# Performance work log

Hardware: AMD Instinct MI355X
Metric: run time of the kernel (lower is better)

Reference implementation:

```python
import jax, jax.numpy as jnp
import numpy as np

N_NODES = 50000
N_EDGES = 600000
D = 128
HIDDEN = 128
N_GRAPHS = 128
N_CLASSES = 10
N_STACKED = 3  # num_layers - 1


def setup_inputs() -> dict:
    key = jax.random.key(0)
    ks = jax.random.split(key, 12)
    s = 1.0 / np.sqrt(HIDDEN)
    inp = {
        "x": jax.random.normal(ks[0], (N_NODES, D), dtype=jnp.float32),
        "edge_index": jax.random.randint(ks[1], (2, N_EDGES), 0, N_NODES, dtype=jnp.int64),
        "batch": jnp.sort(jax.random.randint(ks[2], (N_NODES,), 0, N_GRAPHS, dtype=jnp.int64)),
        "W1": jax.random.normal(ks[3], (D, HIDDEN), dtype=jnp.float32) * s,
        "R1": jax.random.normal(ks[4], (D, HIDDEN), dtype=jnp.float32) * s,
        "b1": jnp.zeros((HIDDEN,), dtype=jnp.float32),
        "Wc": jax.random.normal(ks[5], (N_STACKED, HIDDEN, HIDDEN), dtype=jnp.float32) * s,
        "Rc": jax.random.normal(ks[6], (N_STACKED, HIDDEN, HIDDEN), dtype=jnp.float32) * s,
        "bc": jnp.zeros((N_STACKED, HIDDEN), dtype=jnp.float32),
        "lin1_w": jax.random.normal(ks[7], (HIDDEN, HIDDEN), dtype=jnp.float32) * s,
        "lin1_b": jnp.zeros((HIDDEN,), dtype=jnp.float32),
        "lin2_w": jax.random.normal(ks[8], (HIDDEN, N_CLASSES), dtype=jnp.float32) * s,
        "lin2_b": jnp.zeros((N_CLASSES,), dtype=jnp.float32),
    }
    return inp


def _gcn_norm(edge_index, n_nodes):
    # symmetric GCN normalization coeffs per edge (edge_weight=None -> ones)
    src, dst = edge_index[0], edge_index[1]
    ones = jnp.ones((edge_index.shape[1],), dtype=jnp.float32)
    deg = jax.ops.segment_sum(ones, dst, num_segments=n_nodes)
    dinv = jnp.where(deg > 0, jax.lax.rsqrt(jnp.maximum(deg, 1.0)), 0.0)
    return dinv[src] * dinv[dst]


def _gcs(x, src, dst, norm, W, R, b):
    # GCN aggregation on transformed features + linear skip (root) connection
    h = x @ W                                   # [N, H]
    msg = h[src] * norm[:, None]                # gather + scale, [E, H]
    agg = jax.ops.segment_sum(msg, dst, num_segments=x.shape[0])
    return agg + x @ R + b


def reference(x, edge_index, batch, W1, R1, b1, Wc, Rc, bc,
              lin1_w, lin1_b, lin2_w, lin2_b):
    src, dst = edge_index[0], edge_index[1]
    norm = _gcn_norm(edge_index, x.shape[0])

    h = jax.nn.relu(_gcs(x, src, dst, norm, W1, R1, b1))
    for i in range(N_STACKED):
        h = jax.nn.relu(_gcs(h, src, dst, norm, Wc[i], Rc[i], bc[i]))
    last = h

    # global mean pool over graphs
    sums = jax.ops.segment_sum(h, batch, num_segments=N_GRAPHS)
    cnts = jax.ops.segment_sum(jnp.ones((h.shape[0],), h.dtype), batch,
                               num_segments=N_GRAPHS)
    pooled = sums / jnp.maximum(cnts, 1.0)[:, None]

    g = jax.nn.relu(pooled @ lin1_w + lin1_b)   # dropout is identity in eval mode
    logits = g @ lin2_w + lin2_b
    return jax.nn.log_softmax(logits, axis=-1), last
```

## Files before the change

kernel.cpp:

```cpp
#include <hip/hip_runtime.h>

#define N_NODES  50000
#define N_EDGES  600000
#define DIM      128
#define N_GRAPHS 128
#define N_CLASSES 10
#define NB_SCAN  196


typedef __bf16 bf16x8 __attribute__((ext_vector_type(8)));
typedef float  f32x4  __attribute__((ext_vector_type(4)));

__device__ inline unsigned short f2bf(float f) {
  union { float f; unsigned int i; } u; u.f = f;
  unsigned int r = u.i + 0x7fff + ((u.i >> 16) & 1);
  return (unsigned short)(r >> 16);
}
__device__ inline float bf2f(unsigned short s) {
  union { unsigned int i; float f; } u; u.i = ((unsigned int)s) << 16;
  return u.f;
}
__device__ inline bf16x8 zero8() {
  union { bf16x8 v; unsigned long long q[2]; } u;
  u.q[0] = 0ull; u.q[1] = 0ull;
  return u.v;
}
__device__ inline bf16x8 pack8(float4 lo, float4 hi) {
  union { bf16x8 v; unsigned short s[8]; } u;
  u.s[0] = f2bf(lo.x); u.s[1] = f2bf(lo.y); u.s[2] = f2bf(lo.z); u.s[3] = f2bf(lo.w);
  u.s[4] = f2bf(hi.x); u.s[5] = f2bf(hi.y); u.s[6] = f2bf(hi.z); u.s[7] = f2bf(hi.w);
  return u.v;
}


__global__ __launch_bounds__(256) void k_zero(float* __restrict__ p, int n) {
  int i = blockIdx.x * 256 + threadIdx.x;
  if (i < n) p[i] = 0.f;
}


__global__ __launch_bounds__(256) void k_pack(const float* __restrict__ W1,
                                              const float* __restrict__ R1,
                                              const float* __restrict__ Wc,
                                              const float* __restrict__ Rc,
                                              unsigned short* __restrict__ pk) {
  int mm = blockIdx.y;
  const float* src = (mm == 0) ? W1
                   : (mm < 4)  ? Wc + (size_t)(mm - 1) * DIM * DIM
                   : (mm == 4) ? R1
                               : Rc + (size_t)(mm - 5) * DIM * DIM;
  int idx = blockIdx.x * 256 + threadIdx.x;
  int lane = idx & 63;
  int kc   = (idx >> 6) & 3;
  int nt   = idx >> 8;
  int col  = nt * 16 + (lane & 15);
  int k0   = kc * 32 + (lane >> 4) * 8;
  unsigned short* dst = pk + (size_t)mm * 16384 + (size_t)idx * 8;
  ushort4 u;
  u.x = f2bf(src[(k0 + 0) * DIM + col]);
  u.y = f2bf(src[(k0 + 1) * DIM + col]);
  u.z = f2bf(src[(k0 + 2) * DIM + col]);
  u.w = f2bf(src[(k0 + 3) * DIM + col]);
  *(ushort4*)&dst[0] = u;
  u.x = f2bf(src[(k0 + 4) * DIM + col]);
  u.y = f2bf(src[(k0 + 5) * DIM + col]);
  u.z = f2bf(src[(k0 + 6) * DIM + col]);
  u.w = f2bf(src[(k0 + 7) * DIM + col]);
  *(ushort4*)&dst[4] = u;
}


__global__ __launch_bounds__(256) void k_deg(const int* __restrict__ ei,
                                             int* __restrict__ deg) {
  int e = blockIdx.x * 256 + threadIdx.x;
  if (e < N_EDGES) atomicAdd(&deg[ei[N_EDGES + e]], 1);
}

__global__ __launch_bounds__(256) void k_dinv(const int* __restrict__ deg,
                                              float* __restrict__ dinv) {
  int n = blockIdx.x * 256 + threadIdx.x;
  if (n < N_NODES) {
    int d = deg[n];
    dinv[n] = (d > 0) ? rsqrtf((float)d) : 0.f;
  }
}

__global__ __launch_bounds__(256) void k_bsum(const int* __restrict__ deg,
                                              int* __restrict__ bsum) {
  int i = blockIdx.x * 256 + threadIdx.x;
  int v = (i < N_NODES) ? deg[i] : 0;
  __shared__ int tmp[256];
  int t = threadIdx.x;
  tmp[t] = v;
  __syncthreads();
  for (int off = 128; off > 0; off >>= 1) {
    if (t < off) tmp[t] += tmp[t + off];
    __syncthreads();
  }
  if (t == 0) bsum[blockIdx.x] = tmp[0];
}

__global__ __launch_bounds__(256) void k_bscan(const int* __restrict__ bsum,
                                               int* __restrict__ boff,
                                               int* __restrict__ rowp) {
  int t = threadIdx.x;
  int v = (t < NB_SCAN) ? bsum[t] : 0;
  __shared__ int tmp[256];
  tmp[t] = v;
  __syncthreads();
  for (int off = 1; off < 256; off <<= 1) {
    int add = (t >= off) ? tmp[t - off] : 0;
    __syncthreads();
    tmp[t] += add;
    __syncthreads();
  }
  boff[t] = tmp[t] - v;
  if (t == 0) rowp[N_NODES] = N_EDGES;
}

__global__ __launch_bounds__(256) void k_rowp(const int* __restrict__ deg,
                                              const int* __restrict__ boff,
                                              int* __restrict__ rowp) {
  int i = blockIdx.x * 256 + threadIdx.x;
  int t = threadIdx.x;
  int v = (i < N_NODES) ? deg[i] : 0;
  __shared__ int tmp[256];
  tmp[t] = v;
  __syncthreads();
  for (int off = 1; off < 256; off <<= 1) {
    int add = (t >= off) ? tmp[t - off] : 0;
    __syncthreads();
    tmp[t] += add;
    __syncthreads();
  }
  if (i < N_NODES) rowp[i] = boff[blockIdx.x] + tmp[t] - v;
}

__global__ __launch_bounds__(256) void k_fill(const int* __restrict__ ei,
                                              const int* __restrict__ rowp,
                                              int* __restrict__ cnt,
                                              const float* __restrict__ dinv,
                                              int* __restrict__ csrc,
                                              float* __restrict__ enorm) {
  int e = blockIdx.x * 256 + threadIdx.x;
  if (e < N_EDGES) {
    int s = ei[e];
    int d = ei[N_EDGES + e];
    int p = rowp[d] + atomicAdd(&cnt[d], 1);
    csrc[p] = s;
    enorm[p] = dinv[s] * dinv[d];
  }
}


template<bool AF32, bool LAST>
__global__ __launch_bounds__(256) void k_gemm(const void* __restrict__ act,
                                              const unsigned short* __restrict__ pkW,
                                              const unsigned short* __restrict__ pkR,
                                              const float* __restrict__ bv,
                                              unsigned short* __restrict__ hwb,
                                              unsigned short* __restrict__ skipb,
                                              float* __restrict__ skipf) {
  const int tid  = threadIdx.x;
  const int wave = tid >> 6, lane = tid & 63;
  const int m = lane & 15, q = lane >> 4;
  const int rbase = blockIdx.x * 64 + wave * 16;
  const int arow  = rbase + m;
  const bool aok  = arow < N_NODES;

  bf16x8 a[4];
  if (AF32) {
    const float* xf = (const float*)act;
#pragma unroll
    for (int kc = 0; kc < 4; ++kc) {
      float4 lo = make_float4(0.f, 0.f, 0.f, 0.f);
      float4 hi = make_float4(0.f, 0.f, 0.f, 0.f);
      if (aok) {
        lo = *(const float4*)&xf[arow * DIM + kc * 32 + q * 8];
        hi = *(const float4*)&xf[arow * DIM + kc * 32 + q * 8 + 4];
      }
      a[kc] = pack8(lo, hi);
    }
  } else {
    const unsigned short* xb = (const unsigned short*)act;
#pragma unroll
    for (int kc = 0; kc < 4; ++kc) {
      bf16x8 v = zero8();
      if (aok) v = *(const bf16x8*)&xb[arow * DIM + kc * 32 + q * 8];
      a[kc] = v;
    }
  }

  f32x4 acc[16];
#pragma unroll
  for (int t = 0; t < 16; ++t) acc[t] = (f32x4){0.f, 0.f, 0.f, 0.f};

#pragma unroll
  for (int nt = 0; nt < 8; ++nt) {
    const unsigned short* pw = pkW + ((size_t)(nt * 4) * 64 + lane) * 8;
    const unsigned short* pr = pkR + ((size_t)(nt * 4) * 64 + lane) * 8;
#pragma unroll
    for (int kc = 0; kc < 4; ++kc) {
      bf16x8 bW = *(const bf16x8*)(pw + (size_t)kc * 64 * 8);
      acc[nt] = __builtin_amdgcn_mfma_f32_16x16x32_bf16(a[kc], bW, acc[nt], 0, 0, 0);
    }
#pragma unroll
    for (int kc = 0; kc < 4; ++kc) {
      bf16x8 bR = *(const bf16x8*)(pr + (size_t)kc * 64 * 8);
      acc[8 + nt] = __builtin_amdgcn_mfma_f32_16x16x32_bf16(a[kc], bR, acc[8 + nt], 0, 0, 0);
    }
  }

#pragma unroll
  for (int nt = 0; nt < 8; ++nt) {
    int col = nt * 16 + m;
#pragma unroll
    for (int rg = 0; rg < 4; ++rg) {
      int row = rbase + q * 4 + rg;
      if (row < N_NODES) hwb[row * DIM + col] = f2bf(acc[nt][rg]);
    }
  }
#pragma unroll
  for (int nt = 0; nt < 8; ++nt) {
    int col = nt * 16 + m;
    float bias = bv[col];
#pragma unroll
    for (int rg = 0; rg < 4; ++rg) {
      int row = rbase + q * 4 + rg;
      if (row < N_NODES) {
        float v = acc[8 + nt][rg] + bias;
        if (LAST) skipf[row * DIM + col] = v;
        else      skipb[row * DIM + col] = f2bf(v);
      }
    }
  }
}


template<bool LAST>
__global__ __launch_bounds__(256) void k_agg(const unsigned short* __restrict__ hwb,
                                             const int* __restrict__ rowp,
                                             const int* __restrict__ csrc,
                                             const float* __restrict__ enorm,
                                             unsigned short* __restrict__ actb,
                                             float* __restrict__ actf) {
  int n = blockIdx.x * 8 + (threadIdx.x >> 5);
  if (n >= N_NODES) return;
  int l4 = (threadIdx.x & 31) * 4;
  float4 acc;
  if (LAST) {
    acc = *(const float4*)&actf[n * DIM + l4];
  } else {
    ushort4 s = *(const ushort4*)&actb[n * DIM + l4];
    acc = make_float4(bf2f(s.x), bf2f(s.y), bf2f(s.z), bf2f(s.w));
  }
  int e = rowp[n], e1 = rowp[n + 1];
  for (; e + 4 <= e1; e += 4) {
    int s0 = csrc[e],     s1 = csrc[e + 1], s2 = csrc[e + 2], s3 = csrc[e + 3];
    float w0 = enorm[e],  w1 = enorm[e + 1], w2 = enorm[e + 2], w3 = enorm[e + 3];
    ushort4 u0 = *(const ushort4*)&hwb[s0 * DIM + l4];
    ushort4 u1 = *(const ushort4*)&hwb[s1 * DIM + l4];
    ushort4 u2 = *(const ushort4*)&hwb[s2 * DIM + l4];
    ushort4 u3 = *(const ushort4*)&hwb[s3 * DIM + l4];
    acc.x = fmaf(w0, bf2f(u0.x), fmaf(w1, bf2f(u1.x), fmaf(w2, bf2f(u2.x), fmaf(w3, bf2f(u3.x), acc.x))));
    acc.y = fmaf(w0, bf2f(u0.y), fmaf(w1, bf2f(u1.y), fmaf(w2, bf2f(u2.y), fmaf(w3, bf2f(u3.y), acc.y))));
    acc.z = fmaf(w0, bf2f(u0.z), fmaf(w1, bf2f(u1.z), fmaf(w2, bf2f(u2.z), fmaf(w3, bf2f(u3.z), acc.z))));
    acc.w = fmaf(w0, bf2f(u0.w), fmaf(w1, bf2f(u1.w), fmaf(w2, bf2f(u2.w), fmaf(w3, bf2f(u3.w), acc.w))));
  }
  for (; e < e1; ++e) {
    int s0 = csrc[e];
    float w0 = enorm[e];
    ushort4 u0 = *(const ushort4*)&hwb[s0 * DIM + l4];
    acc.x = fmaf(w0, bf2f(u0.x), acc.x);
    acc.y = fmaf(w0, bf2f(u0.y), acc.y);
    acc.z = fmaf(w0, bf2f(u0.z), acc.z);
    acc.w = fmaf(w0, bf2f(u0.w), acc.w);
  }
  acc.x = fmaxf(acc.x, 0.f);
  acc.y = fmaxf(acc.y, 0.f);
  acc.z = fmaxf(acc.z, 0.f);
  acc.w = fmaxf(acc.w, 0.f);
  if (LAST) {
    *(float4*)&actf[n * DIM + l4] = acc;
  } else {
    ushort4 o;
    o.x = f2bf(acc.x); o.y = f2bf(acc.y); o.z = f2bf(acc.z); o.w = f2bf(acc.w);
    *(ushort4*)&actb[n * DIM + l4] = o;
  }
}


__global__ __launch_bounds__(1024) void k_pool2(const float* __restrict__ h,
                                                const int* __restrict__ batch,
                                                float* __restrict__ pooled) {
  int g = blockIdx.x;
  int t = threadIdx.x;
  __shared__ int sb[2];
  if (t < 2) {
    int target = g + t;
    int lo = 0, hi = N_NODES;
    while (lo < hi) {
      int mid = (lo + hi) >> 1;
      if (batch[mid] < target) lo = mid + 1; else hi = mid;
    }
    sb[t] = lo;
  }
  __syncthreads();
  int start = sb[0], end = sb[1];
  int c = t & 127, rg = t >> 7;
  float acc = 0.f;
  for (int r = start + rg; r < end; r += 8) acc += h[r * DIM + c];
  __shared__ float sp[8][DIM];
  sp[rg][c] = acc;
  __syncthreads();
  if (rg == 0) {
    float tot = acc;
#pragma unroll
    for (int i = 1; i < 8; ++i) tot += sp[i][c];
    float cnt = fmaxf((float)(end - start), 1.f);
    pooled[g * DIM + c] = tot / cnt;
  }
}


__global__ __launch_bounds__(128) void k_mlp1(const float* __restrict__ pooled,
                                              const float* __restrict__ w,
                                              const float* __restrict__ bias,
                                              float* __restrict__ g1) {
  int g = blockIdx.x, t = threadIdx.x;
  __shared__ float sp[DIM];
  sp[t] = pooled[g * DIM + t];
  __syncthreads();
  float acc = bias[t];
#pragma unroll 4
  for (int k = 0; k < DIM; ++k) acc = fmaf(sp[k], w[k * DIM + t], acc);
  g1[g * DIM + t] = fmaxf(acc, 0.f);
}

__global__ __launch_bounds__(128) void k_mlp2(const float* __restrict__ g1,
                                              const float* __restrict__ w,
                                              const float* __restrict__ bias,
                                              float* __restrict__ out) {
  int g = threadIdx.x;
  float l[N_CLASSES];
#pragma unroll
  for (int c = 0; c < N_CLASSES; ++c) l[c] = bias[c];
  for (int k = 0; k < DIM; ++k) {
    float gv = g1[g * DIM + k];
#pragma unroll
    for (int c = 0; c < N_CLASSES; ++c) l[c] = fmaf(gv, w[k * N_CLASSES + c], l[c]);
  }
  float m = l[0];
#pragma unroll
  for (int c = 1; c < N_CLASSES; ++c) m = fmaxf(m, l[c]);
  float s = 0.f;
#pragma unroll
  for (int c = 0; c < N_CLASSES; ++c) s += expf(l[c] - m);
  float lse = logf(s) + m;
#pragma unroll
  for (int c = 0; c < N_CLASSES; ++c) out[g * N_CLASSES + c] = l[c] - lse;
}


extern "C" void kernel_launch(void* const* d_in, const int* in_sizes, int n_in,
                              void* d_out, int out_size, void* d_ws, size_t ws_size,
                              hipStream_t stream) {
  const float* x     = (const float*)d_in[0];
  const int* ei      = (const int*)d_in[1];
  const int* batch   = (const int*)d_in[2];
  const float* W1  = (const float*)d_in[3];
  const float* R1  = (const float*)d_in[4];
  const float* b1  = (const float*)d_in[5];
  const float* Wc  = (const float*)d_in[6];
  const float* Rc  = (const float*)d_in[7];
  const float* bc  = (const float*)d_in[8];
  const float* l1w = (const float*)d_in[9];
  const float* l1b = (const float*)d_in[10];
  const float* l2w = (const float*)d_in[11];
  const float* l2b = (const float*)d_in[12];

  float* out   = (float*)d_out;
  float* dlast = out + N_GRAPHS * N_CLASSES;

  float* ws    = (float*)d_ws;
  unsigned short* hwb  = (unsigned short*)ws;
  unsigned short* actb = (unsigned short*)(ws + 3200000);
  int*   deg   = (int*)(ws + 6400000);
  int*   cnt   = (int*)(ws + 6450000);
  float* pooled= ws + 6500000;
  float* dinv  = ws + 6516384;
  int*   rowp  = (int*)(ws + 6566384);
  int*   csrc  = (int*)(ws + 6616400);
  float* enorm = ws + 7216400;
  float* g1    = ws + 7816400;
  unsigned short* pk = (unsigned short*)(ws + 7832784);
  int*   bsum  = (int*)(ws + 7898320);
  int*   boff  = (int*)(ws + 7898576);

  k_zero<<<(100000 + 255) / 256, 256, 0, stream>>>(ws + 6400000, 100000);

  k_pack<<<dim3(8, 8), 256, 0, stream>>>(W1, R1, Wc, Rc, pk);
  k_deg <<<(N_EDGES + 255) / 256, 256, 0, stream>>>(ei, deg);
  k_dinv<<<(N_NODES + 255) / 256, 256, 0, stream>>>(deg, dinv);
  k_bsum<<<NB_SCAN, 256, 0, stream>>>(deg, bsum);
  k_bscan<<<1, 256, 0, stream>>>(bsum, boff, rowp);
  k_rowp<<<NB_SCAN, 256, 0, stream>>>(deg, boff, rowp);
  k_fill<<<(N_EDGES + 255) / 256, 256, 0, stream>>>(ei, rowp, cnt, dinv, csrc, enorm);

  const int NGB = (N_NODES + 63) / 64;
  const int NAB = (N_NODES + 7) / 8;

  k_gemm<true, false><<<NGB, 256, 0, stream>>>(
      x, pk + 0 * 16384, pk + 4 * 16384, b1, hwb, actb, nullptr);
  k_agg<false><<<NAB, 256, 0, stream>>>(hwb, rowp, csrc, enorm, actb, nullptr);

  for (int l = 1; l <= 2; ++l) {
    k_gemm<false, false><<<NGB, 256, 0, stream>>>(
        actb, pk + (size_t)l * 16384, pk + (size_t)(4 + l) * 16384,
        bc + (size_t)(l - 1) * DIM, hwb, actb, nullptr);
    k_agg<false><<<NAB, 256, 0, stream>>>(hwb, rowp, csrc, enorm, actb, nullptr);
  }

  k_gemm<false, true><<<NGB, 256, 0, stream>>>(
      actb, pk + 3 * 16384, pk + 7 * 16384, bc + 2 * DIM, hwb, nullptr, dlast);
  k_agg<true><<<NAB, 256, 0, stream>>>(hwb, rowp, csrc, enorm, nullptr, dlast);

  k_pool2<<<N_GRAPHS, 1024, 0, stream>>>(dlast, batch, pooled);
  k_mlp1<<<N_GRAPHS, 128, 0, stream>>>(pooled, l1w, l1b, g1);
  k_mlp2<<<1, N_GRAPHS, 0, stream>>>(g1, l2w, l2b, out);
}
```

Measured before the change: 402.8 us.

## Fuse aggregation into next layer's GEMM and pad CSR rows to four edges

Each layer's neighbor aggregation (plus skip, bias, ReLU) is now done inside the following GEMM kernel, with the result staged in LDS. This removes the round trip of the activation tensor through global memory and cuts the number of launches, using ping-pong h buffers and a separate skip buffer. CSR rows are padded to multiples of four with zero-filled csrc/enorm entries so the edge loop can use int4/float4 loads with no scalar tail. Zeroing, weight packing and the dinv/bsum kernels are also merged to drop more launches. The cost is a larger zeroed workspace and gathers that may be less latency-tolerant with 64-row blocks.

```diff
diff --git a/kernel.cpp b/kernel.cpp
--- a/kernel.cpp
+++ b/kernel.cpp
@@ -6,6 +6,8 @@
 #define N_GRAPHS 128
 #define N_CLASSES 10
 #define NB_SCAN  196
+#define LDSW     136
+#define NZB      6266
 
 
 typedef __bf16 bf16x8 __attribute__((ext_vector_type(8)));
@@ -19,11 +21,6 @@
 __device__ inline float bf2f(unsigned short s) {
   union { unsigned int i; float f; } u; u.i = ((unsigned int)s) << 16;
   return u.f;
-}
-__device__ inline bf16x8 zero8() {
-  union { bf16x8 v; unsigned long long q[2]; } u;
-  u.q[0] = 0ull; u.q[1] = 0ull;
-  return u.v;
 }
 __device__ inline bf16x8 pack8(float4 lo, float4 hi) {
   union { bf16x8 v; unsigned short s[8]; } u;
@@ -33,23 +30,24 @@
 }
 
 
-__global__ __launch_bounds__(256) void k_zero(float* __restrict__ p, int n) {
-  int i = blockIdx.x * 256 + threadIdx.x;
-  if (i < n) p[i] = 0.f;
-}
-
-
-__global__ __launch_bounds__(256) void k_pack(const float* __restrict__ W1,
+__global__ __launch_bounds__(256) void k_prep(float* __restrict__ zbase,
+                                              const float* __restrict__ W1,
                                               const float* __restrict__ R1,
                                               const float* __restrict__ Wc,
                                               const float* __restrict__ Rc,
                                               unsigned short* __restrict__ pk) {
-  int mm = blockIdx.y;
+  if (blockIdx.x < NZB) {
+    int i = blockIdx.x * 256 + threadIdx.x;
+    if (i < 1604000) zbase[i] = 0.f;
+    return;
+  }
+  int pb = blockIdx.x - NZB;
+  int mm = pb >> 3, sub = pb & 7;
   const float* src = (mm == 0) ? W1
                    : (mm < 4)  ? Wc + (size_t)(mm - 1) * DIM * DIM
                    : (mm == 4) ? R1
                                : Rc + (size_t)(mm - 5) * DIM * DIM;
-  int idx = blockIdx.x * 256 + threadIdx.x;
+  int idx = sub * 256 + threadIdx.x;
   int lane = idx & 63;
   int kc   = (idx >> 6) & 3;
   int nt   = idx >> 8;
@@ -76,22 +74,16 @@
   if (e < N_EDGES) atomicAdd(&deg[ei[N_EDGES + e]], 1);
 }
 
-__global__ __launch_bounds__(256) void k_dinv(const int* __restrict__ deg,
-                                              float* __restrict__ dinv) {
-  int n = blockIdx.x * 256 + threadIdx.x;
-  if (n < N_NODES) {
-    int d = deg[n];
-    dinv[n] = (d > 0) ? rsqrtf((float)d) : 0.f;
-  }
-}
-
-__global__ __launch_bounds__(256) void k_bsum(const int* __restrict__ deg,
-                                              int* __restrict__ bsum) {
+__global__ __launch_bounds__(256) void k_dinvsum(const int* __restrict__ deg,
+                                                 float* __restrict__ dinv,
+                                                 int* __restrict__ bsum) {
   int i = blockIdx.x * 256 + threadIdx.x;
-  int v = (i < N_NODES) ? deg[i] : 0;
+  int t = threadIdx.x;
+  int d = (i < N_NODES) ? deg[i] : 0;
+  if (i < N_NODES) dinv[i] = (d > 0) ? rsqrtf((float)d) : 0.f;
+  int dp = (d + 3) & ~3;
   __shared__ int tmp[256];
-  int t = threadIdx.x;
-  tmp[t] = v;
+  tmp[t] = dp;
   __syncthreads();
   for (int off = 128; off > 0; off >>= 1) {
     if (t < off) tmp[t] += tmp[t + off];
@@ -115,7 +107,7 @@
     __syncthreads();
   }
   boff[t] = tmp[t] - v;
-  if (t == 0) rowp[N_NODES] = N_EDGES;
+  if (t == 255) rowp[N_NODES] = tmp[255];
 }
 
 __global__ __launch_bounds__(256) void k_rowp(const int* __restrict__ deg,
@@ -123,9 +115,9 @@
                                               int* __restrict__ rowp) {
   int i = blockIdx.x * 256 + threadIdx.x;
   int t = threadIdx.x;
-  int v = (i < N_NODES) ? deg[i] : 0;
+  int dp = (i < N_NODES) ? ((deg[i] + 3) & ~3) : 0;
   __shared__ int tmp[256];
-  tmp[t] = v;
+  tmp[t] = dp;
   __syncthreads();
   for (int off = 1; off < 256; off <<= 1) {
     int add = (t >= off) ? tmp[t - off] : 0;
@@ -133,7 +125,7 @@
     tmp[t] += add;
     __syncthreads();
   }
-  if (i < N_NODES) rowp[i] = boff[blockIdx.x] + tmp[t] - v;
+  if (i < N_NODES) rowp[i] = boff[blockIdx.x] + tmp[t] - dp;
 }
 
 __global__ __launch_bounds__(256) void k_fill(const int* __restrict__ ei,
@@ -153,14 +145,12 @@
 }
 
 
-template<bool AF32, bool LAST>
-__global__ __launch_bounds__(256) void k_gemm(const void* __restrict__ act,
-                                              const unsigned short* __restrict__ pkW,
-                                              const unsigned short* __restrict__ pkR,
-                                              const float* __restrict__ bv,
-                                              unsigned short* __restrict__ hwb,
-                                              unsigned short* __restrict__ skipb,
-                                              float* __restrict__ skipf) {
+__global__ __launch_bounds__(256) void k_gemm0(const float* __restrict__ xf,
+                                               const unsigned short* __restrict__ pkW,
+                                               const unsigned short* __restrict__ pkR,
+                                               const float* __restrict__ bv,
+                                               unsigned short* __restrict__ hwb,
+                                               unsigned short* __restrict__ skipb) {
   const int tid  = threadIdx.x;
   const int wave = tid >> 6, lane = tid & 63;
   const int m = lane & 15, q = lane >> 4;
@@ -169,26 +159,15 @@
   const bool aok  = arow < N_NODES;
 
   bf16x8 a[4];
-  if (AF32) {
-    const float* xf = (const float*)act;
-#pragma unroll
-    for (int kc = 0; kc < 4; ++kc) {
-      float4 lo = make_float4(0.f, 0.f, 0.f, 0.f);
-      float4 hi = make_float4(0.f, 0.f, 0.f, 0.f);
-      if (aok) {
-        lo = *(const float4*)&xf[arow * DIM + kc * 32 + q * 8];
-        hi = *(const float4*)&xf[arow * DIM + kc * 32 + q * 8 + 4];
-      }
-      a[kc] = pack8(lo, hi);
-    }
-  } else {
-    const unsigned short* xb = (const unsigned short*)act;
-#pragma unroll
-    for (int kc = 0; kc < 4; ++kc) {
-      bf16x8 v = zero8();
-      if (aok) v = *(const bf16x8*)&xb[arow * DIM + kc * 32 + q * 8];
-      a[kc] = v;
-    }
+#pragma unroll
+  for (int kc = 0; kc < 4; ++kc) {
+    float4 lo = make_float4(0.f, 0.f, 0.f, 0.f);
+    float4 hi = make_float4(0.f, 0.f, 0.f, 0.f);
+    if (aok) {
+      lo = *(const float4*)&xf[arow * DIM + kc * 32 + q * 8];
+      hi = *(const float4*)&xf[arow * DIM + kc * 32 + q * 8 + 4];
+    }
+    a[kc] = pack8(lo, hi);
   }
 
   f32x4 acc[16];
@@ -214,12 +193,98 @@
 #pragma unroll
   for (int nt = 0; nt < 8; ++nt) {
     int col = nt * 16 + m;
+    float bias = bv[col];
 #pragma unroll
     for (int rg = 0; rg < 4; ++rg) {
       int row = rbase + q * 4 + rg;
-      if (row < N_NODES) hwb[row * DIM + col] = f2bf(acc[nt][rg]);
-    }
-  }
+      if (row < N_NODES) {
+        hwb[row * DIM + col]   = f2bf(acc[nt][rg]);
+        skipb[row * DIM + col] = f2bf(acc[8 + nt][rg] + bias);
+      }
+    }
+  }
+}
+
+
+template<bool LAST>
+__global__ __launch_bounds__(256) void k_aggemm(const unsigned short* __restrict__ hin,
+                                                const int* __restrict__ rowp,
+                                                const int* __restrict__ csrc,
+                                                const float* __restrict__ enorm,
+                                                const unsigned short* __restrict__ pkW,
+                                                const unsigned short* __restrict__ pkR,
+                                                const float* __restrict__ bv,
+                                                unsigned short* __restrict__ hout,
+                                                unsigned short* __restrict__ skipb,
+                                                float* __restrict__ skipf) {
+  __shared__ unsigned short xs[64 * LDSW];
+  const int tid = threadIdx.x;
+  const int row0 = blockIdx.x * 64;
+
+  {
+    int hw = tid >> 5;
+    int l4 = (tid & 31) * 4;
+    for (int rnd = 0; rnd < 8; ++rnd) {
+      int n = row0 + rnd * 8 + hw;
+      float4 acc = make_float4(0.f, 0.f, 0.f, 0.f);
+      if (n < N_NODES) {
+        ushort4 s = *(const ushort4*)&skipb[n * DIM + l4];
+        acc = make_float4(bf2f(s.x), bf2f(s.y), bf2f(s.z), bf2f(s.w));
+        int e0 = rowp[n], e1 = rowp[n + 1];
+        for (int e = e0; e < e1; e += 4) {
+          int4   cs = *(const int4*)&csrc[e];
+          float4 wv = *(const float4*)&enorm[e];
+          ushort4 u0 = *(const ushort4*)&hin[cs.x * DIM + l4];
+          ushort4 u1 = *(const ushort4*)&hin[cs.y * DIM + l4];
+          ushort4 u2 = *(const ushort4*)&hin[cs.z * DIM + l4];
+          ushort4 u3 = *(const ushort4*)&hin[cs.w * DIM + l4];
+          acc.x = fmaf(wv.x, bf2f(u0.x), fmaf(wv.y, bf2f(u1.x), fmaf(wv.z, bf2f(u2.x), fmaf(wv.w, bf2f(u3.x), acc.x))));
+          acc.y = fmaf(wv.x, bf2f(u0.y), fmaf(wv.y, bf2f(u1.y), fmaf(wv.z, bf2f(u2.y), fmaf(wv.w, bf2f(u3.y), acc.y))));
+          acc.z = fmaf(wv.x, bf2f(u0.z), fmaf(wv.y, bf2f(u1.z), fmaf(wv.z, bf2f(u2.z), fmaf(wv.w, bf2f(u3.z), acc.z))));
+          acc.w = fmaf(wv.x, bf2f(u0.w), fmaf(wv.y, bf2f(u1.w), fmaf(wv.z, bf2f(u2.w), fmaf(wv.w, bf2f(u3.w), acc.w))));
+        }
+        acc.x = fmaxf(acc.x, 0.f);
+        acc.y = fmaxf(acc.y, 0.f);
+        acc.z = fmaxf(acc.z, 0.f);
+        acc.w = fmaxf(acc.w, 0.f);
+      }
+      int r = rnd * 8 + hw;
+      ushort4 o;
+      o.x = f2bf(acc.x); o.y = f2bf(acc.y); o.z = f2bf(acc.z); o.w = f2bf(acc.w);
+      *(ushort4*)&xs[r * LDSW + l4] = o;
+    }
+  }
+  __syncthreads();
+
+  const int wave = tid >> 6, lane = tid & 63;
+  const int m = lane & 15, q = lane >> 4;
+  const int rbase = row0 + wave * 16;
+
+  bf16x8 a[4];
+#pragma unroll
+  for (int kc = 0; kc < 4; ++kc)
+    a[kc] = *(const bf16x8*)&xs[(wave * 16 + m) * LDSW + kc * 32 + q * 8];
+
+  f32x4 acc[16];
+#pragma unroll
+  for (int t = 0; t < 16; ++t) acc[t] = (f32x4){0.f, 0.f, 0.f, 0.f};
+
+#pragma unroll
+  for (int nt = 0; nt < 8; ++nt) {
+    const unsigned short* pw = pkW + ((size_t)(nt * 4) * 64 + lane) * 8;
+    const unsigned short* pr = pkR + ((size_t)(nt * 4) * 64 + lane) * 8;
+#pragma unroll
+    for (int kc = 0; kc < 4; ++kc) {
+      bf16x8 bW = *(const bf16x8*)(pw + (size_t)kc * 64 * 8);
+      acc[nt] = __builtin_amdgcn_mfma_f32_16x16x32_bf16(a[kc], bW, acc[nt], 0, 0, 0);
+    }
+#pragma unroll
+    for (int kc = 0; kc < 4; ++kc) {
+      bf16x8 bR = *(const bf16x8*)(pr + (size_t)kc * 64 * 8);
+      acc[8 + nt] = __builtin_amdgcn_mfma_f32_16x16x32_bf16(a[kc], bR, acc[8 + nt], 0, 0, 0);
+    }
+  }
+
 #pragma unroll
   for (int nt = 0; nt < 8; ++nt) {
     int col = nt * 16 + m;
@@ -228,6 +293,7 @@
     for (int rg = 0; rg < 4; ++rg) {
       int row = rbase + q * 4 + rg;
       if (row < N_NODES) {
+        hout[row * DIM + col] = f2bf(acc[nt][rg]);
         float v = acc[8 + nt][rg] + bias;
         if (LAST) skipf[row * DIM + col] = v;
         else      skipb[row * DIM + col] = f2bf(v);
@@ -237,56 +303,33 @@
 }
 
 
-template<bool LAST>
-__global__ __launch_bounds__(256) void k_agg(const unsigned short* __restrict__ hwb,
-                                             const int* __restrict__ rowp,
-                                             const int* __restrict__ csrc,
-                                             const float* __restrict__ enorm,
-                                             unsigned short* __restrict__ actb,
-                                             float* __restrict__ actf) {
+__global__ __launch_bounds__(256) void k_aggF(const unsigned short* __restrict__ hwb,
+                                              const int* __restrict__ rowp,
+                                              const int* __restrict__ csrc,
+                                              const float* __restrict__ enorm,
+                                              float* __restrict__ actf) {
   int n = blockIdx.x * 8 + (threadIdx.x >> 5);
   if (n >= N_NODES) return;
   int l4 = (threadIdx.x & 31) * 4;
-  float4 acc;
-  if (LAST) {
-    acc = *(const float4*)&actf[n * DIM + l4];
-  } else {
-    ushort4 s = *(const ushort4*)&actb[n * DIM + l4];
-    acc = make_float4(bf2f(s.x), bf2f(s.y), bf2f(s.z), bf2f(s.w));
-  }
-  int e = rowp[n], e1 = rowp[n + 1];
-  for (; e + 4 <= e1; e += 4) {
-    int s0 = csrc[e],     s1 = csrc[e + 1], s2 = csrc[e + 2], s3 = csrc[e + 3];
-    float w0 = enorm[e],  w1 = enorm[e + 1], w2 = enorm[e + 2], w3 = enorm[e + 3];
-    ushort4 u0 = *(const ushort4*)&hwb[s0 * DIM + l4];
-    ushort4 u1 = *(const ushort4*)&hwb[s1 * DIM + l4];
-    ushort4 u2 = *(const ushort4*)&hwb[s2 * DIM + l4];
-    ushort4 u3 = *(const ushort4*)&hwb[s3 * DIM + l4];
-    acc.x = fmaf(w0, bf2f(u0.x), fmaf(w1, bf2f(u1.x), fmaf(w2, bf2f(u2.x), fmaf(w3, bf2f(u3.x), acc.x))));
-    acc.y = fmaf(w0, bf2f(u0.y), fmaf(w1, bf2f(u1.y), fmaf(w2, bf2f(u2.y), fmaf(w3, bf2f(u3.y), acc.y))));
-    acc.z = fmaf(w0, bf2f(u0.z), fmaf(w1, bf2f(u1.z), fmaf(w2, bf2f(u2.z), fmaf(w3, bf2f(u3.z), acc.z))));
-    acc.w = fmaf(w0, bf2f(u0.w), fmaf(w1, bf2f(u1.w), fmaf(w2, bf2f(u2.w), fmaf(w3, bf2f(u3.w), acc.w))));
-  }
-  for (; e < e1; ++e) {
-    int s0 = csrc[e];
-    float w0 = enorm[e];
-    ushort4 u0 = *(const ushort4*)&hwb[s0 * DIM + l4];
-    acc.x = fmaf(w0, bf2f(u0.x), acc.x);
-    acc.y = fmaf(w0, bf2f(u0.y), acc.y);
-    acc.z = fmaf(w0, bf2f(u0.z), acc.z);
-    acc.w = fmaf(w0, bf2f(u0.w), acc.w);
+  float4 acc = *(const float4*)&actf[n * DIM + l4];
+  int e0 = rowp[n], e1 = rowp[n + 1];
+  for (int e = e0; e < e1; e += 4) {
+    int4   cs = *(const int4*)&csrc[e];
+    float4 wv = *(const float4*)&enorm[e];
+    ushort4 u0 = *(const ushort4*)&hwb[cs.x * DIM + l4];
+    ushort4 u1 = *(const ushort4*)&hwb[cs.y * DIM + l4];
+    ushort4 u2 = *(const ushort4*)&hwb[cs.z * DIM + l4];
+    ushort4 u3 = *(const ushort4*)&hwb[cs.w * DIM + l4];
+    acc.x = fmaf(wv.x, bf2f(u0.x), fmaf(wv.y, bf2f(u1.x), fmaf(wv.z, bf2f(u2.x), fmaf(wv.w, bf2f(u3.x), acc.x))));
+    acc.y = fmaf(wv.x, bf2f(u0.y), fmaf(wv.y, bf2f(u1.y), fmaf(wv.z, bf2f(u2.y), fmaf(wv.w, bf2f(u3.y), acc.y))));
+    acc.z = fmaf(wv.x, bf2f(u0.z), fmaf(wv.y, bf2f(u1.z), fmaf(wv.z, bf2f(u2.z), fmaf(wv.w, bf2f(u3.z), acc.z))));
+    acc.w = fmaf(wv.x, bf2f(u0.w), fmaf(wv.y, bf2f(u1.w), fmaf(wv.z, bf2f(u2.w), fmaf(wv.w, bf2f(u3.w), acc.w))));
   }
   acc.x = fmaxf(acc.x, 0.f);
   acc.y = fmaxf(acc.y, 0.f);
   acc.z = fmaxf(acc.z, 0.f);
   acc.w = fmaxf(acc.w, 0.f);
-  if (LAST) {
-    *(float4*)&actf[n * DIM + l4] = acc;
-  } else {
-    ushort4 o;
-    o.x = f2bf(acc.x); o.y = f2bf(acc.y); o.z = f2bf(acc.z); o.w = f2bf(acc.w);
-    *(ushort4*)&actb[n * DIM + l4] = o;
-  }
+  *(float4*)&actf[n * DIM + l4] = acc;
 }
 
 
@@ -382,27 +425,25 @@
   float* out   = (float*)d_out;
   float* dlast = out + N_GRAPHS * N_CLASSES;
 
-  float* ws    = (float*)d_ws;
-  unsigned short* hwb  = (unsigned short*)ws;
-  unsigned short* actb = (unsigned short*)(ws + 3200000);
-  int*   deg   = (int*)(ws + 6400000);
-  int*   cnt   = (int*)(ws + 6450000);
-  float* pooled= ws + 6500000;
-  float* dinv  = ws + 6516384;
-  int*   rowp  = (int*)(ws + 6566384);
-  int*   csrc  = (int*)(ws + 6616400);
-  float* enorm = ws + 7216400;
-  float* g1    = ws + 7816400;
-  unsigned short* pk = (unsigned short*)(ws + 7832784);
-  int*   bsum  = (int*)(ws + 7898320);
-  int*   boff  = (int*)(ws + 7898576);
-
-  k_zero<<<(100000 + 255) / 256, 256, 0, stream>>>(ws + 6400000, 100000);
-
-  k_pack<<<dim3(8, 8), 256, 0, stream>>>(W1, R1, Wc, Rc, pk);
+  float* ws = (float*)d_ws;
+  unsigned short* h0    = (unsigned short*)ws;
+  unsigned short* h1    = (unsigned short*)(ws + 3200000);
+  unsigned short* skipb = (unsigned short*)(ws + 6400000);
+  int*   deg   = (int*)(ws + 9600000);
+  int*   cnt   = (int*)(ws + 9650000);
+  int*   csrc  = (int*)(ws + 9700000);
+  float* enorm = ws + 10452000;
+  float* dinv  = ws + 11204000;
+  int*   rowp  = (int*)(ws + 11254000);
+  float* pooled= ws + 11304016;
+  float* g1    = ws + 11320400;
+  unsigned short* pk = (unsigned short*)(ws + 11336784);
+  int*   bsum  = (int*)(ws + 11402320);
+  int*   boff  = (int*)(ws + 11402576);
+
+  k_prep<<<NZB + 64, 256, 0, stream>>>(ws + 9600000, W1, R1, Wc, Rc, pk);
   k_deg <<<(N_EDGES + 255) / 256, 256, 0, stream>>>(ei, deg);
-  k_dinv<<<(N_NODES + 255) / 256, 256, 0, stream>>>(deg, dinv);
-  k_bsum<<<NB_SCAN, 256, 0, stream>>>(deg, bsum);
+  k_dinvsum<<<NB_SCAN, 256, 0, stream>>>(deg, dinv, bsum);
   k_bscan<<<1, 256, 0, stream>>>(bsum, boff, rowp);
   k_rowp<<<NB_SCAN, 256, 0, stream>>>(deg, boff, rowp);
   k_fill<<<(N_EDGES + 255) / 256, 256, 0, stream>>>(ei, rowp, cnt, dinv, csrc, enorm);
@@ -410,20 +451,14 @@
   const int NGB = (N_NODES + 63) / 64;
   const int NAB = (N_NODES + 7) / 8;
 
-  k_gemm<true, false><<<NGB, 256, 0, stream>>>(
-      x, pk + 0 * 16384, pk + 4 * 16384, b1, hwb, actb, nullptr);
-  k_agg<false><<<NAB, 256, 0, stream>>>(hwb, rowp, csrc, enorm, actb, nullptr);
-
-  for (int l = 1; l <= 2; ++l) {
-    k_gemm<false, false><<<NGB, 256, 0, stream>>>(
-        actb, pk + (size_t)l * 16384, pk + (size_t)(4 + l) * 16384,
-        bc + (size_t)(l - 1) * DIM, hwb, actb, nullptr);
-    k_agg<false><<<NAB, 256, 0, stream>>>(hwb, rowp, csrc, enorm, actb, nullptr);
-  }
-
-  k_gemm<false, true><<<NGB, 256, 0, stream>>>(
-      actb, pk + 3 * 16384, pk + 7 * 16384, bc + 2 * DIM, hwb, nullptr, dlast);
-  k_agg<true><<<NAB, 256, 0, stream>>>(hwb, rowp, csrc, enorm, nullptr, dlast);
+  k_gemm0<<<NGB, 256, 0, stream>>>(x, pk + 0 * 16384, pk + 4 * 16384, b1, h0, skipb);
+  k_aggemm<false><<<NGB, 256, 0, stream>>>(h0, rowp, csrc, enorm,
+      pk + 1 * 16384, pk + 5 * 16384, bc + 0 * DIM, h1, skipb, nullptr);
+  k_aggemm<false><<<NGB, 256, 0, stream>>>(h1, rowp, csrc, enorm,
+      pk + 2 * 16384, pk + 6 * 16384, bc + 1 * DIM, h0, skipb, nullptr);
+  k_aggemm<true><<<NGB, 256, 0, stream>>>(h0, rowp, csrc, enorm,
+      pk + 3 * 16384, pk + 7 * 16384, bc + 2 * DIM, h1, skipb, dlast);
+  k_aggF<<<NAB, 256, 0, stream>>>(h1, rowp, csrc, enorm, dlast);
 
   k_pool2<<<N_GRAPHS, 1024, 0, stream>>>(dlast, batch, pooled);
   k_mlp1<<<N_GRAPHS, 128, 0, stream>>>(pooled, l1w, l1b, g1);
```

Measured after the change: 394.4 us. 2.1% less time.
